# Kernel optimization log

Hardware: AMD Instinct MI355X
Metric: run time of the kernel (lower is better)

## Reference

```python
import jax, jax.numpy as jnp
import numpy as np


def gcn_conv(x, edge_index, edge_weight, W, b):
    """PyG GCNConv: add self-loops (weight 1), symmetric degree norm, aggregate, linear."""
    N = x.shape[0]
    loop = jnp.arange(N, dtype=edge_index.dtype)
    src = jnp.concatenate([edge_index[0], loop])
    dst = jnp.concatenate([edge_index[1], loop])
    ew = jnp.concatenate([edge_weight, jnp.ones((N,), dtype=x.dtype)])
    deg = jax.ops.segment_sum(ew, dst, num_segments=N)
    dinv = jnp.where(deg > 0, jax.lax.rsqrt(deg), 0.0)
    norm = dinv[src] * ew * dinv[dst]            # [E+N]
    h = x @ W                                    # [N, out] transform first
    msg = h[src] * norm[:, None]                 # gather + scale
    out = jax.ops.segment_sum(msg, dst, num_segments=N)  # scatter-add
    return out + b


def l2norm(x, eps=1e-12):
    n = jnp.sqrt(jnp.sum(x * x, axis=-1, keepdims=True))
    return x / jnp.maximum(n, eps)


def setup_inputs() -> dict:
    key = jax.random.key(0)
    ks = jax.random.split(key, 16)
    N_net, E_net, N_dag, E_dag = 100000, 600000, 50000, 400000
    D_net, D_dag, H_net, H_dag = 128, 128, 128, 128
    s = lambda fan_in: 1.0 / np.sqrt(fan_in)
    return {
        "net_feat": jax.random.normal(ks[0], (N_net, D_net), jnp.float32),
        "net_edge_index": jax.random.randint(ks[1], (2, E_net), 0, N_net, jnp.int32),
        "net_edge_weights": jax.random.uniform(ks[2], (E_net,), jnp.float32),
        "dag_feat": jax.random.normal(ks[3], (N_dag, D_dag), jnp.float32),
        "dag_edge_index": jax.random.randint(ks[4], (2, E_dag), 0, N_dag, jnp.int32),
        "dag_edge_weights": jax.random.uniform(ks[5], (E_dag,), jnp.float32),
        "W_net": jax.random.normal(ks[6], (D_net, H_net), jnp.float32) * s(D_net),
        "b_net": jnp.zeros((H_net,), jnp.float32),
        "W_dag": jax.random.normal(ks[7], (D_dag, H_dag), jnp.float32) * s(D_dag),
        "b_dag": jnp.zeros((H_dag,), jnp.float32),
        "W1": jax.random.normal(ks[8], (H_net + H_dag, 64), jnp.float32) * s(H_net + H_dag),
        "b1": jnp.zeros((64,), jnp.float32),
        "W2": jax.random.normal(ks[9], (64, 1), jnp.float32) * s(64),
        "b2": jnp.zeros((1,), jnp.float32),
    }


def reference(net_feat, net_edge_index, net_edge_weights,
              dag_feat, dag_edge_index, dag_edge_weights,
              W_net, b_net, W_dag, b_dag, W1, b1, W2, b2):
    net_emb = jax.nn.relu(gcn_conv(net_feat, net_edge_index, net_edge_weights, W_net, b_net))
    dag_emb = jax.nn.relu(gcn_conv(dag_feat, dag_edge_index, dag_edge_weights, W_dag, b_dag))
    # normalize == True
    net_emb = l2norm(net_emb)
    dag_emb = l2norm(dag_emb)
    # net_batch/dag_batch are None: mean over nodes -> single state value
    net_vec = net_emb.mean(axis=0)
    dag_vec = dag_emb.mean(axis=0)
    combined = jnp.concatenate([net_vec, dag_vec], axis=-1)
    h = jax.nn.relu(combined @ W1 + b1)
    state_val = h @ W2 + b2
    return state_val
```

## Files before the change

kernel.cpp:

```cpp
#include <hip/hip_runtime.h>

#define FD 128
#define PAD 48
#define WSCALE 16777216.0f
#define WINV   5.9604645e-8f

__device__ inline unsigned short f2bf(float f) {
    unsigned u = __float_as_uint(f);
    return (unsigned short)((u + 0x7fffu + ((u >> 16) & 1u)) >> 16);
}
__device__ inline void bf4_to_f32(uint2 u, float& a, float& b, float& c, float& d) {
    a = __uint_as_float(u.x << 16);
    b = __uint_as_float(u.x & 0xffff0000u);
    c = __uint_as_float(u.y << 16);
    d = __uint_as_float(u.y & 0xffff0000u);
}
__device__ inline float pc_to_dinv(unsigned long long pv) {
    return rsqrtf((float)(pv & 0xffffffffull) * WINV + 1.0f);
}

__global__ __launch_bounds__(256) void bucket_both(
        const int* __restrict__ ei_n, const float* __restrict__ ew_n,
        unsigned long long* __restrict__ pc_n, int2* __restrict__ el_n,
        int E_n, int GBn,
        const int* __restrict__ ei_d, const float* __restrict__ ew_d,
        unsigned long long* __restrict__ pc_d, int2* __restrict__ el_d,
        int E_d) {
    int b = blockIdx.x;
    const int* ei; const float* ew; unsigned long long* pc; int2* el; int E, e;
    if (b < GBn) { ei = ei_n; ew = ew_n; pc = pc_n; el = el_n; E = E_n;
                   e = b * 256 + threadIdx.x; }
    else         { ei = ei_d; ew = ew_d; pc = pc_d; el = el_d; E = E_d;
                   e = (b - GBn) * 256 + threadIdx.x; }
    if (e < E) {
        int src = ei[e];
        int dst = ei[E + e];
        float w = ew[e];
        unsigned long long val =
            (1ull << 32) |
            (unsigned long long)(unsigned int)__float2uint_rn(w * WSCALE);
        unsigned long long old = atomicAdd(&pc[dst], val);
        unsigned int pos = (unsigned int)(old >> 32);
        if (pos < PAD)
            el[(size_t)dst * PAD + pos] = make_int2(src, __float_as_int(w));
    }
}

__global__ __launch_bounds__(256) void gemm_both(
        const float* __restrict__ X_n, const float* __restrict__ W_n,
        const unsigned long long* __restrict__ pc_n, unsigned short* __restrict__ hs_n,
        int N_n, int Gn,
        const float* __restrict__ X_d, const float* __restrict__ W_d,
        const unsigned long long* __restrict__ pc_d, unsigned short* __restrict__ hs_d,
        int N_d) {
    __shared__ float As[128][36];
    __shared__ float Wt[32][FD];

    const float *X, *W; const unsigned long long* pc; unsigned short* hs; int N, r0;
    if (blockIdx.x < Gn) { X = X_n; W = W_n; pc = pc_n; hs = hs_n; N = N_n;
                           r0 = blockIdx.x * 128; }
    else                 { X = X_d; W = W_d; pc = pc_d; hs = hs_d; N = N_d;
                           r0 = (blockIdx.x - Gn) * 128; }

    const int tid = threadIdx.x;
    const int tx = tid & 15;
    const int ty = tid >> 4;

    float acc[8][8] = {};

    for (int kt = 0; kt < FD; kt += 32) {
        __syncthreads();
        #pragma unroll
        for (int i2 = 0; i2 < 4; i2++) {
            int idx = tid + i2 * 256;
            int k = idx >> 5, c4 = idx & 31;
            *(float4*)&Wt[k][c4 * 4] =
                *(const float4*)&W[(size_t)(kt + k) * FD + c4 * 4];
        }
        #pragma unroll
        for (int i2 = 0; i2 < 4; i2++) {
            int idx = tid + i2 * 256;
            int row_l = idx >> 3, kq = idx & 7;
            int row = r0 + row_l;
            float4 a = make_float4(0.f, 0.f, 0.f, 0.f);
            if (row < N) a = *(const float4*)&X[(size_t)row * FD + kt + kq * 4];
            *(float4*)&As[row_l][kq * 4] = a;
        }
        __syncthreads();
        #pragma unroll
        for (int k4 = 0; k4 < 8; k4++) {
            float4 wl[4], wh[4];
            #pragma unroll
            for (int kk = 0; kk < 4; kk++) {
                wl[kk] = *(const float4*)&Wt[k4 * 4 + kk][tx * 4];
                wh[kk] = *(const float4*)&Wt[k4 * 4 + kk][64 + tx * 4];
            }
            #pragma unroll
            for (int r = 0; r < 8; r++) {
                float4 av = *(const float4*)&As[r * 16 + ty][k4 * 4];
                float ak[4] = {av.x, av.y, av.z, av.w};
                #pragma unroll
                for (int kk = 0; kk < 4; kk++) {
                    acc[r][0] = fmaf(ak[kk], wl[kk].x, acc[r][0]);
                    acc[r][1] = fmaf(ak[kk], wl[kk].y, acc[r][1]);
                    acc[r][2] = fmaf(ak[kk], wl[kk].z, acc[r][2]);
                    acc[r][3] = fmaf(ak[kk], wl[kk].w, acc[r][3]);
                    acc[r][4] = fmaf(ak[kk], wh[kk].x, acc[r][4]);
                    acc[r][5] = fmaf(ak[kk], wh[kk].y, acc[r][5]);
                    acc[r][6] = fmaf(ak[kk], wh[kk].z, acc[r][6]);
                    acc[r][7] = fmaf(ak[kk], wh[kk].w, acc[r][7]);
                }
            }
        }
    }

    #pragma unroll
    for (int r = 0; r < 8; r++) {
        int row = r0 + r * 16 + ty;
        if (row < N) {
            float dv = pc_to_dinv(pc[row]);
            ushort4 lo, hi;
            lo.x = f2bf(acc[r][0] * dv); lo.y = f2bf(acc[r][1] * dv);
            lo.z = f2bf(acc[r][2] * dv); lo.w = f2bf(acc[r][3] * dv);
            hi.x = f2bf(acc[r][4] * dv); hi.y = f2bf(acc[r][5] * dv);
            hi.z = f2bf(acc[r][6] * dv); hi.w = f2bf(acc[r][7] * dv);
            *(ushort4*)&hs[(size_t)row * FD + tx * 4]      = lo;
            *(ushort4*)&hs[(size_t)row * FD + 64 + tx * 4] = hi;
        }
    }
}

__global__ __launch_bounds__(256) void gather_reduce_both(
        const unsigned short* __restrict__ hs_n,
        const unsigned long long* __restrict__ pc_n, const int2* __restrict__ el_n,
        const float* __restrict__ b_n, int N_n,
        const unsigned short* __restrict__ hs_d,
        const unsigned long long* __restrict__ pc_d, const int2* __restrict__ el_d,
        const float* __restrict__ b_d, int N_d,
        float* __restrict__ vec) {
    __shared__ float accw[8][2 * FD];
    const int tid  = threadIdx.x;
    const int hw   = tid >> 5;
    const int sl   = tid & 31;

    float4 bbn = *(const float4*)&b_n[sl * 4];
    float4 bbd = *(const float4*)&b_d[sl * 4];
    float an0 = 0.f, an1 = 0.f, an2 = 0.f, an3 = 0.f;
    float ad0 = 0.f, ad1 = 0.f, ad2 = 0.f, ad3 = 0.f;

    const int total = N_n + N_d;
    const int stride = gridDim.x * 8;
    for (int t = blockIdx.x * 8 + hw; t < total; t += stride) {
        const bool isn = t < N_n;
        const int i = isn ? t : t - N_n;
        const unsigned short* hs = isn ? hs_n : hs_d;
        const unsigned long long* pc = isn ? pc_n : pc_d;
        const int2* el = (isn ? el_n : el_d) + (size_t)i * PAD;

        unsigned long long pv = pc[i];
        int cnt = (int)(pv >> 32);
        if (cnt > PAD) cnt = PAD;
        float dv = pc_to_dinv(pv);

        int2 my = (sl < cnt) ? el[sl] : make_int2(0, 0);

        float s0, s1, s2, s3;
        bf4_to_f32(*(const uint2*)&hs[(size_t)i * FD + sl * 4], s0, s1, s2, s3);
        float x0 = s0 * dv, x1 = s1 * dv, x2 = s2 * dv, x3 = s3 * dv;

        int lim = cnt < 32 ? cnt : 32;
        int j = 0;
        for (; j + 4 <= lim; j += 4) {
            int   q0 = __shfl(my.x, j,     32);
            float w0 = __int_as_float(__shfl(my.y, j,     32)) * dv;
            int   q1 = __shfl(my.x, j + 1, 32);
            float w1 = __int_as_float(__shfl(my.y, j + 1, 32)) * dv;
            int   q2 = __shfl(my.x, j + 2, 32);
            float w2 = __int_as_float(__shfl(my.y, j + 2, 32)) * dv;
            int   q3 = __shfl(my.x, j + 3, 32);
            float w3 = __int_as_float(__shfl(my.y, j + 3, 32)) * dv;
            uint2 u0 = *(const uint2*)&hs[(size_t)q0 * FD + sl * 4];
            uint2 u1 = *(const uint2*)&hs[(size_t)q1 * FD + sl * 4];
            uint2 u2 = *(const uint2*)&hs[(size_t)q2 * FD + sl * 4];
            uint2 u3 = *(const uint2*)&hs[(size_t)q3 * FD + sl * 4];
            float a, b2, c, d;
            bf4_to_f32(u0, a, b2, c, d);
            x0 = fmaf(a, w0, x0); x1 = fmaf(b2, w0, x1);
            x2 = fmaf(c, w0, x2); x3 = fmaf(d, w0, x3);
            bf4_to_f32(u1, a, b2, c, d);
            x0 = fmaf(a, w1, x0); x1 = fmaf(b2, w1, x1);
            x2 = fmaf(c, w1, x2); x3 = fmaf(d, w1, x3);
            bf4_to_f32(u2, a, b2, c, d);
            x0 = fmaf(a, w2, x0); x1 = fmaf(b2, w2, x1);
            x2 = fmaf(c, w2, x2); x3 = fmaf(d, w2, x3);
            bf4_to_f32(u3, a, b2, c, d);
            x0 = fmaf(a, w3, x0); x1 = fmaf(b2, w3, x1);
            x2 = fmaf(c, w3, x2); x3 = fmaf(d, w3, x3);
        }
        for (; j < lim; j++) {
            int   q = __shfl(my.x, j, 32);
            float w = __int_as_float(__shfl(my.y, j, 32)) * dv;
            uint2 u = *(const uint2*)&hs[(size_t)q * FD + sl * 4];
            float a, b2, c, d;
            bf4_to_f32(u, a, b2, c, d);
            x0 = fmaf(a, w, x0); x1 = fmaf(b2, w, x1);
            x2 = fmaf(c, w, x2); x3 = fmaf(d, w, x3);
        }
        for (; j < cnt; j++) {
            int2 p = el[j];
            float w = __int_as_float(p.y) * dv;
            uint2 u = *(const uint2*)&hs[(size_t)p.x * FD + sl * 4];
            float a, b2, c, d;
            bf4_to_f32(u, a, b2, c, d);
            x0 = fmaf(a, w, x0); x1 = fmaf(b2, w, x1);
            x2 = fmaf(c, w, x2); x3 = fmaf(d, w, x3);
        }

        float4 bb = isn ? bbn : bbd;
        x0 = fmaxf(x0 + bb.x, 0.f);
        x1 = fmaxf(x1 + bb.y, 0.f);
        x2 = fmaxf(x2 + bb.z, 0.f);
        x3 = fmaxf(x3 + bb.w, 0.f);
        float ss = fmaf(x0, x0, fmaf(x1, x1, fmaf(x2, x2, x3 * x3)));
        #pragma unroll
        for (int o = 16; o; o >>= 1) ss += __shfl_xor(ss, o);
        float inv = 1.0f / fmaxf(sqrtf(ss), 1e-12f);
        if (isn) {
            an0 = fmaf(x0, inv, an0); an1 = fmaf(x1, inv, an1);
            an2 = fmaf(x2, inv, an2); an3 = fmaf(x3, inv, an3);
        } else {
            ad0 = fmaf(x0, inv, ad0); ad1 = fmaf(x1, inv, ad1);
            ad2 = fmaf(x2, inv, ad2); ad3 = fmaf(x3, inv, ad3);
        }
    }
    accw[hw][sl * 4 + 0] = an0;
    accw[hw][sl * 4 + 1] = an1;
    accw[hw][sl * 4 + 2] = an2;
    accw[hw][sl * 4 + 3] = an3;
    accw[hw][FD + sl * 4 + 0] = ad0;
    accw[hw][FD + sl * 4 + 1] = ad1;
    accw[hw][FD + sl * 4 + 2] = ad2;
    accw[hw][FD + sl * 4 + 3] = ad3;
    __syncthreads();
    {
        float s = accw[0][tid] + accw[1][tid] + accw[2][tid] + accw[3][tid]
                + accw[4][tid] + accw[5][tid] + accw[6][tid] + accw[7][tid];
        unsafeAtomicAdd(&vec[tid], s);
    }
}

__global__ __launch_bounds__(256) void final_kernel(
        const float* __restrict__ vec,
        const float* __restrict__ W1, const float* __restrict__ b1,
        const float* __restrict__ W2, const float* __restrict__ b2,
        float* __restrict__ out, float invNnet, float invNdag) {
    __shared__ float part[4][64];
    int j = threadIdx.x & 63;
    int q = threadIdx.x >> 6;
    float h = 0.f;
    for (int k = q * 64; k < q * 64 + 64; k++) {
        float sc = (k < 128) ? invNnet : invNdag;
        h = fmaf(vec[k] * sc, W1[k * 64 + j], h);
    }
    part[q][j] = h;
    __syncthreads();
    if (threadIdx.x < 64) {
        float hh = b1[j] + part[0][j] + part[1][j] + part[2][j] + part[3][j];
        hh = fmaxf(hh, 0.f);
        float p = hh * W2[j];
        #pragma unroll
        for (int o = 32; o; o >>= 1) p += __shfl_xor(p, o);
        if (j == 0) out[0] = p + b2[0];
    }
}

extern "C" void kernel_launch(void* const* d_in, const int* in_sizes, int n_in,
                              void* d_out, int out_size, void* d_ws, size_t ws_size,
                              hipStream_t stream) {
    const float* net_feat = (const float*)d_in[0];
    const int*   net_ei   = (const int*)d_in[1];
    const float* net_ew   = (const float*)d_in[2];
    const float* dag_feat = (const float*)d_in[3];
    const int*   dag_ei   = (const int*)d_in[4];
    const float* dag_ew   = (const float*)d_in[5];
    const float* W_net    = (const float*)d_in[6];
    const float* b_net    = (const float*)d_in[7];
    const float* W_dag    = (const float*)d_in[8];
    const float* b_dag    = (const float*)d_in[9];
    const float* W1       = (const float*)d_in[10];
    const float* b1       = (const float*)d_in[11];
    const float* W2       = (const float*)d_in[12];
    const float* b2       = (const float*)d_in[13];

    const int N_net = in_sizes[0] / FD;
    const int E_net = in_sizes[2];
    const int N_dag = in_sizes[3] / FD;
    const int E_dag = in_sizes[5];
    const int GBn = (E_net + 255) / 256, GBd = (E_dag + 255) / 256;
    const int Gn  = (N_net + 127) / 128, Gd  = (N_dag + 127) / 128;

    char* w = (char*)d_ws;
    size_t o = 0;
    unsigned short* hs_net = (unsigned short*)(w + o); o += (size_t)2 * N_net * FD;
    unsigned short* hs_dag = (unsigned short*)(w + o); o += (size_t)2 * N_dag * FD;
    unsigned long long* pc_net = (unsigned long long*)(w + o); o += (size_t)8 * N_net;
    unsigned long long* pc_dag = (unsigned long long*)(w + o); o += (size_t)8 * N_dag;
    float* vec = (float*)(w + o); o += 256 * 4;
    size_t zbytes = (size_t)8 * (N_net + N_dag) + 256 * 4;
    int2* elist_net = (int2*)(w + o); o += (size_t)8 * N_net * PAD;
    int2* elist_dag = (int2*)(w + o); o += (size_t)8 * N_dag * PAD;

    hipMemsetAsync(pc_net, 0, zbytes, stream);

    bucket_both<<<GBn + GBd, 256, 0, stream>>>(
        net_ei, net_ew, pc_net, elist_net, E_net, GBn,
        dag_ei, dag_ew, pc_dag, elist_dag, E_dag);

    gemm_both<<<Gn + Gd, 256, 0, stream>>>(net_feat, W_net, pc_net, hs_net, N_net, Gn,
                                           dag_feat, W_dag, pc_dag, hs_dag, N_dag);

    gather_reduce_both<<<2048, 256, 0, stream>>>(
        hs_net, pc_net, elist_net, b_net, N_net,
        hs_dag, pc_dag, elist_dag, b_dag, N_dag, vec);

    final_kernel<<<1, 256, 0, stream>>>(vec, W1, b1, W2, b2, (float*)d_out,
                                        1.0f / (float)N_net, 1.0f / (float)N_dag);
}
```

Before: 380.8 us.

## Replace FP32 SIMT GEMM with split-bf16 MFMA GEMM using prepacked weights

New measurement: 346.7 us. 8.9% less time.

```diff
diff --git a/kernel.cpp b/kernel.cpp
--- a/kernel.cpp
+++ b/kernel.cpp
@@ -4,6 +4,9 @@
 #define PAD 48
 #define WSCALE 16777216.0f
 #define WINV   5.9604645e-8f
+
+typedef __attribute__((ext_vector_type(8))) short short8;
+typedef __attribute__((ext_vector_type(4))) float f32x4;
 
 __device__ inline unsigned short f2bf(float f) {
     unsigned u = __float_as_uint(f);
@@ -18,15 +21,46 @@
 __device__ inline float pc_to_dinv(unsigned long long pv) {
     return rsqrtf((float)(pv & 0xffffffffull) * WINV + 1.0f);
 }
-
-__global__ __launch_bounds__(256) void bucket_both(
+__device__ inline void split1(float x, unsigned short& h, unsigned short& l) {
+    unsigned u = __float_as_uint(x);
+    unsigned hh = (u + 0x7fffu + ((u >> 16) & 1u)) >> 16;
+    float r = x - __uint_as_float(hh << 16);
+    unsigned u2 = __float_as_uint(r);
+    h = (unsigned short)hh;
+    l = (unsigned short)((u2 + 0x7fffu + ((u2 >> 16) & 1u)) >> 16);
+}
+
+__global__ __launch_bounds__(256) void bucket_pack(
         const int* __restrict__ ei_n, const float* __restrict__ ew_n,
         unsigned long long* __restrict__ pc_n, int2* __restrict__ el_n,
         int E_n, int GBn,
         const int* __restrict__ ei_d, const float* __restrict__ ew_d,
         unsigned long long* __restrict__ pc_d, int2* __restrict__ el_d,
-        int E_d) {
+        int E_d,
+        const float* __restrict__ Wn, const float* __restrict__ Wd,
+        unsigned short* __restrict__ Wpack) {
     int b = blockIdx.x;
+    int packStart = (int)gridDim.x - 16;
+    if (b >= packStart) {
+        int p = b - packStart;
+        int graph = p >> 3, pb = p & 7;
+        const float* W = graph ? Wd : Wn;
+        int c  = threadIdx.x & 127;
+        int hh = threadIdx.x >> 7;
+        int k0 = pb * 16 + hh * 8;
+        short8 hv, lv;
+        #pragma unroll
+        for (int j = 0; j < 8; j++) {
+            unsigned short hq, lq;
+            split1(W[(k0 + j) * FD + c], hq, lq);
+            hv[j] = (short)hq; lv[j] = (short)lq;
+        }
+        char* dst = (char*)Wpack + graph * 65536
+                  + c * 256 + 16 * ((k0 >> 3) ^ (c & 15));
+        *(short8*)dst = hv;
+        *(short8*)(dst + 32768) = lv;
+        return;
+    }
     const int* ei; const float* ew; unsigned long long* pc; int2* el; int E, e;
     if (b < GBn) { ei = ei_n; ew = ew_n; pc = pc_n; el = el_n; E = E_n;
                    e = b * 256 + threadIdx.x; }
@@ -46,86 +80,113 @@
     }
 }
 
-__global__ __launch_bounds__(256) void gemm_both(
-        const float* __restrict__ X_n, const float* __restrict__ W_n,
-        const unsigned long long* __restrict__ pc_n, unsigned short* __restrict__ hs_n,
-        int N_n, int Gn,
-        const float* __restrict__ X_d, const float* __restrict__ W_d,
-        const unsigned long long* __restrict__ pc_d, unsigned short* __restrict__ hs_d,
-        int N_d) {
-    __shared__ float As[128][36];
-    __shared__ float Wt[32][FD];
-
-    const float *X, *W; const unsigned long long* pc; unsigned short* hs; int N, r0;
-    if (blockIdx.x < Gn) { X = X_n; W = W_n; pc = pc_n; hs = hs_n; N = N_n;
-                           r0 = blockIdx.x * 128; }
-    else                 { X = X_d; W = W_d; pc = pc_d; hs = hs_d; N = N_d;
-                           r0 = (blockIdx.x - Gn) * 128; }
-
-    const int tid = threadIdx.x;
-    const int tx = tid & 15;
-    const int ty = tid >> 4;
-
-    float acc[8][8] = {};
-
-    for (int kt = 0; kt < FD; kt += 32) {
-        __syncthreads();
-        #pragma unroll
-        for (int i2 = 0; i2 < 4; i2++) {
-            int idx = tid + i2 * 256;
-            int k = idx >> 5, c4 = idx & 31;
-            *(float4*)&Wt[k][c4 * 4] =
-                *(const float4*)&W[(size_t)(kt + k) * FD + c4 * 4];
-        }
-        #pragma unroll
-        for (int i2 = 0; i2 < 4; i2++) {
-            int idx = tid + i2 * 256;
-            int row_l = idx >> 3, kq = idx & 7;
-            int row = r0 + row_l;
-            float4 a = make_float4(0.f, 0.f, 0.f, 0.f);
-            if (row < N) a = *(const float4*)&X[(size_t)row * FD + kt + kq * 4];
-            *(float4*)&As[row_l][kq * 4] = a;
-        }
-        __syncthreads();
-        #pragma unroll
-        for (int k4 = 0; k4 < 8; k4++) {
-            float4 wl[4], wh[4];
+__global__ __launch_bounds__(256) void gemm_mfma(
+        const float* __restrict__ X_n, const unsigned long long* __restrict__ pc_n,
+        unsigned short* __restrict__ hs_n, int N_n, int Gn,
+        const float* __restrict__ X_d, const unsigned long long* __restrict__ pc_d,
+        unsigned short* __restrict__ hs_d, int N_d,
+        const unsigned short* __restrict__ Wpack) {
+    __shared__ unsigned short WL[2][128][128];
+
+    const float* X; const unsigned long long* pc; unsigned short* hs; int N, r0;
+    const char* wsrc;
+    if (blockIdx.x < Gn) { X = X_n; pc = pc_n; hs = hs_n; N = N_n;
+                           r0 = blockIdx.x * 128; wsrc = (const char*)Wpack; }
+    else                 { X = X_d; pc = pc_d; hs = hs_d; N = N_d;
+                           r0 = (blockIdx.x - Gn) * 128;
+                           wsrc = (const char*)Wpack + 65536; }
+
+    const int tid  = threadIdx.x;
+    const int w    = tid >> 6;
+    const int lane = tid & 63;
+    const int c15  = lane & 15;
+    const int g    = lane >> 4;
+
+    {
+        const float4* s4 = (const float4*)wsrc;
+        float4* d4 = (float4*)WL;
+        #pragma unroll
+        for (int i = 0; i < 16; i++) d4[tid + i * 256] = s4[tid + i * 256];
+    }
+    __syncthreads();
+
+    f32x4 acc[2][8] = {};
+
+    const int row0 = r0 + 32 * w + c15;
+    const float* x0p = X + (size_t)row0 * FD;
+    const float* x1p = x0p + 16 * FD;
+    const bool v0 = row0 < N, v1 = (row0 + 16) < N;
+
+    #pragma unroll
+    for (int kt = 0; kt < 4; kt++) {
+        const int ko = 32 * kt + 8 * g;
+        float4 a0 = {}, a1 = {}, c0 = {}, c1 = {};
+        if (v0) { a0 = *(const float4*)(x0p + ko); c0 = *(const float4*)(x0p + ko + 4); }
+        if (v1) { a1 = *(const float4*)(x1p + ko); c1 = *(const float4*)(x1p + ko + 4); }
+        short8 ah0, al0, ah1, al1;
+        {
+            float xx[8] = {a0.x, a0.y, a0.z, a0.w, c0.x, c0.y, c0.z, c0.w};
             #pragma unroll
-            for (int kk = 0; kk < 4; kk++) {
-                wl[kk] = *(const float4*)&Wt[k4 * 4 + kk][tx * 4];
-                wh[kk] = *(const float4*)&Wt[k4 * 4 + kk][64 + tx * 4];
+            for (int j = 0; j < 8; j++) {
+                unsigned short hq, lq; split1(xx[j], hq, lq);
+                ah0[j] = (short)hq; al0[j] = (short)lq;
             }
+        }
+        {
+            float xx[8] = {a1.x, a1.y, a1.z, a1.w, c1.x, c1.y, c1.z, c1.w};
             #pragma unroll
-            for (int r = 0; r < 8; r++) {
-                float4 av = *(const float4*)&As[r * 16 + ty][k4 * 4];
-                float ak[4] = {av.x, av.y, av.z, av.w};
-                #pragma unroll
-                for (int kk = 0; kk < 4; kk++) {
-                    acc[r][0] = fmaf(ak[kk], wl[kk].x, acc[r][0]);
-                    acc[r][1] = fmaf(ak[kk], wl[kk].y, acc[r][1]);
-                    acc[r][2] = fmaf(ak[kk], wl[kk].z, acc[r][2]);
-                    acc[r][3] = fmaf(ak[kk], wl[kk].w, acc[r][3]);
-                    acc[r][4] = fmaf(ak[kk], wh[kk].x, acc[r][4]);
-                    acc[r][5] = fmaf(ak[kk], wh[kk].y, acc[r][5]);
-                    acc[r][6] = fmaf(ak[kk], wh[kk].z, acc[r][6]);
-                    acc[r][7] = fmaf(ak[kk], wh[kk].w, acc[r][7]);
-                }
+            for (int j = 0; j < 8; j++) {
+                unsigned short hq, lq; split1(xx[j], hq, lq);
+                ah1[j] = (short)hq; al1[j] = (short)lq;
             }
         }
-    }
-
+
+        const char* bbase = (const char*)WL + c15 * 256
+                          + 16 * (((unsigned)(g + 4 * kt)) ^ (unsigned)c15);
+        #pragma unroll
+        for (int cf = 0; cf < 8; cf++) {
+            short8 bh = *(const short8*)(bbase + cf * 4096);
+            short8 bl = *(const short8*)(bbase + cf * 4096 + 32768);
+            acc[0][cf] = __builtin_amdgcn_mfma_f32_16x16x32_bf16(ah0, bh, acc[0][cf], 0, 0, 0);
+            acc[1][cf] = __builtin_amdgcn_mfma_f32_16x16x32_bf16(ah1, bh, acc[1][cf], 0, 0, 0);
+            acc[0][cf] = __builtin_amdgcn_mfma_f32_16x16x32_bf16(al0, bh, acc[0][cf], 0, 0, 0);
+            acc[1][cf] = __builtin_amdgcn_mfma_f32_16x16x32_bf16(al1, bh, acc[1][cf], 0, 0, 0);
+            acc[0][cf] = __builtin_amdgcn_mfma_f32_16x16x32_bf16(ah0, bl, acc[0][cf], 0, 0, 0);
+            acc[1][cf] = __builtin_amdgcn_mfma_f32_16x16x32_bf16(ah1, bl, acc[1][cf], 0, 0, 0);
+        }
+    }
+
+    __syncthreads();
+    unsigned short* OT = (unsigned short*)WL;
     #pragma unroll
-    for (int r = 0; r < 8; r++) {
-        int row = r0 + r * 16 + ty;
+    for (int rf = 0; rf < 2; rf++) {
+        float dv[4];
+        #pragma unroll
+        for (int r = 0; r < 4; r++) {
+            int row = r0 + 32 * w + 16 * rf + 4 * g + r;
+            dv[r] = pc_to_dinv(row < N ? pc[row] : 0ull);
+        }
+        #pragma unroll
+        for (int cf = 0; cf < 8; cf++) {
+            #pragma unroll
+            for (int r = 0; r < 4; r++) {
+                int lrow = 32 * w + 16 * rf + 4 * g + r;
+                unsigned byteo = (unsigned)(lrow * 256)
+                               + (unsigned)((32 * cf + 2 * c15) ^ ((lrow & 15) << 4));
+                *(unsigned short*)((char*)OT + byteo) = f2bf(acc[rf][cf][r] * dv[r]);
+            }
+        }
+    }
+    __syncthreads();
+    #pragma unroll
+    for (int p = 0; p < 8; p++) {
+        int idx  = p * 256 + tid;
+        int lrow = idx >> 4, ch = idx & 15;
+        int row  = r0 + lrow;
         if (row < N) {
-            float dv = pc_to_dinv(pc[row]);
-            ushort4 lo, hi;
-            lo.x = f2bf(acc[r][0] * dv); lo.y = f2bf(acc[r][1] * dv);
-            lo.z = f2bf(acc[r][2] * dv); lo.w = f2bf(acc[r][3] * dv);
-            hi.x = f2bf(acc[r][4] * dv); hi.y = f2bf(acc[r][5] * dv);
-            hi.z = f2bf(acc[r][6] * dv); hi.w = f2bf(acc[r][7] * dv);
-            *(ushort4*)&hs[(size_t)row * FD + tx * 4]      = lo;
-            *(ushort4*)&hs[(size_t)row * FD + 64 + tx * 4] = hi;
+            uint4 v = *(const uint4*)((const char*)WL + lrow * 256
+                                      + 16 * (ch ^ (lrow & 15)));
+            *(uint4*)&hs[(size_t)row * FD + ch * 8] = v;
         }
     }
 }
@@ -309,15 +370,18 @@
     size_t zbytes = (size_t)8 * (N_net + N_dag) + 256 * 4;
     int2* elist_net = (int2*)(w + o); o += (size_t)8 * N_net * PAD;
     int2* elist_dag = (int2*)(w + o); o += (size_t)8 * N_dag * PAD;
+    unsigned short* Wpack = (unsigned short*)(w + o); o += 131072;
 
     hipMemsetAsync(pc_net, 0, zbytes, stream);
 
-    bucket_both<<<GBn + GBd, 256, 0, stream>>>(
+    bucket_pack<<<GBn + GBd + 16, 256, 0, stream>>>(
         net_ei, net_ew, pc_net, elist_net, E_net, GBn,
-        dag_ei, dag_ew, pc_dag, elist_dag, E_dag);
-
-    gemm_both<<<Gn + Gd, 256, 0, stream>>>(net_feat, W_net, pc_net, hs_net, N_net, Gn,
-                                           dag_feat, W_dag, pc_dag, hs_dag, N_dag);
+        dag_ei, dag_ew, pc_dag, elist_dag, E_dag,
+        W_net, W_dag, Wpack);
+
+    gemm_mfma<<<Gn + Gd, 256, 0, stream>>>(
+        net_feat, pc_net, hs_net, N_net, Gn,
+        dag_feat, pc_dag, hs_dag, N_dag, Wpack);
 
     gather_reduce_both<<<2048, 256, 0, stream>>>(
         hs_net, pc_net, elist_net, b_net, N_net,
```
